# Kernel tuning notes

Hardware: AMD Instinct MI355X
Metric: run time of the kernel (lower is better)

The kernel has to match this reference:

```python
import jax, jax.numpy as jnp
import numpy as np

B, NPG, H, D = 8, 6250, 4, 128   # graphs, nodes/graph, heads, hidden
N = B * NPG                       # 50000 nodes total
E = 400000                        # edges
VOCAB = 10000


def setup_inputs() -> dict:
    key = jax.random.key(0)
    ks = jax.random.split(key, 12)
    p = lambda k, shape: jax.random.normal(k, shape, dtype=jnp.float32) * 0.05
    return {
        "node_ids": jax.random.randint(ks[0], (N,), 0, VOCAB),
        "src": jax.random.randint(ks[1], (E,), 0, N),
        "dst": jax.random.randint(ks[2], (E,), 0, N),
        "emb": p(ks[3], (VOCAB, D)),
        "W_src": p(ks[4], (D, H * D)), "b_src": jnp.zeros((H * D,), jnp.float32),
        "W_dst": p(ks[5], (D, H * D)), "b_dst": jnp.zeros((H * D,), jnp.float32),
        "attn": p(ks[6], (H, D)),
        "W_res": p(ks[7], (D, H * D)), "b_res": jnp.zeros((H * D,), jnp.float32),
        "W_gc": p(ks[8], (D, D)), "b_gc": jnp.zeros((D,), jnp.float32),
        "W_mlp": p(ks[9], (3 * D, 1)), "b_mlp": jnp.zeros((1,), jnp.float32),
    }


def _leaky(x, s):
    return jnp.where(x >= 0, x, s * x)


def _maxpool(feat):
    # dgl.max_nodes: per-graph max over nodes -> [B, feat_dim]
    return jnp.max(feat.reshape(B, NPG, -1), axis=1)


def _gatv2(x, src, dst, W_src, b_src, W_dst, b_dst, attn, W_res, b_res):
    # DGL GATv2Conv (share_weights=False, residual=True, eval mode -> no dropout)
    hs = (x @ W_src + b_src).reshape(N, H, D)
    hd = (x @ W_dst + b_dst).reshape(N, H, D)
    e = _leaky(hs[src] + hd[dst], 0.2)              # [E,H,D]
    logits = jnp.einsum('ehd,hd->eh', e, attn)      # [E,H]
    m = jax.ops.segment_max(logits, dst, num_segments=N)
    ex = jnp.exp(logits - m[dst])
    denom = jax.ops.segment_sum(ex, dst, num_segments=N)
    alpha = ex / denom[dst]                          # edge softmax per dst/head
    rst = jax.ops.segment_sum(hs[src] * alpha[..., None], dst, num_segments=N)
    rst = rst + (x @ W_res + b_res).reshape(N, H, D)
    return _leaky(rst, 0.01)                         # nn.LeakyReLU() activation


def _graphconv(x, src, dst, W, b):
    # DGL GraphConv norm='both', allow_zero_in_degree=True, LeakyReLU activation
    ones = jnp.ones((E,), x.dtype)
    dout = jnp.clip(jax.ops.segment_sum(ones, src, num_segments=N), 1.0, None)
    din = jnp.clip(jax.ops.segment_sum(ones, dst, num_segments=N), 1.0, None)
    h = x * jax.lax.rsqrt(dout)[:, None]
    agg = jax.ops.segment_sum(h[src], dst, num_segments=N)
    h = agg * jax.lax.rsqrt(din)[:, None]
    return _leaky(h @ W + b, 0.01)


def reference(node_ids, src, dst, emb, W_src, b_src, W_dst, b_dst, attn,
              W_res, b_res, W_gc, b_gc, W_mlp, b_mlp):
    feat = emb[node_ids]                             # featurize_nodes
    pools = [_maxpool(feat)]
    res = _gatv2(feat, src, dst, W_src, b_src, W_dst, b_dst, attn,
                 W_res, b_res).mean(axis=1)          # mean over heads -> [N,D]
    pools.append(_maxpool(res))
    res = _graphconv(res, src, dst, W_gc, b_gc)
    pools.append(_maxpool(res))
    agg = jnp.concatenate(pools, axis=1)             # [B, 3D]
    # reward_predictor_block_two: ReLU -> (Dropout eval) -> Linear(3D, 1)
    return jax.nn.relu(agg) @ W_mlp + b_mlp          # BCE logits [B,1]
```

## Files before the change

kernel.cpp:

```cpp
#include <hip/hip_runtime.h>
#include <float.h>
#include <math.h>

#define Bg   8
#define NPGc 6250
#define Hh   4
#define Dd   128
#define Nn   50000
#define Ee   400000
#define HDd  512
#define WNf  1536
#define NCHUNK 49

typedef unsigned short ushort_t;
typedef __attribute__((ext_vector_type(8))) short bf16x8;
typedef __attribute__((ext_vector_type(4))) float f32x4;

__device__ __forceinline__ void atomicMaxF(float* addr, float val) {
    if (val >= 0.0f) atomicMax((int*)addr, __float_as_int(val));
    else             atomicMin((unsigned int*)addr, __float_as_uint(val));
}

__device__ __forceinline__ ushort_t f2bf(float x) {
    unsigned u = __float_as_uint(x);
    unsigned r = (u + 0x7FFFu + ((u >> 16) & 1u)) >> 16;
    return (ushort_t)r;
}

__device__ __forceinline__ void bf2x2(unsigned u, float& lo, float& hi) {
    lo = __uint_as_float(u << 16);
    hi = __uint_as_float(u & 0xFFFF0000u);
}

__global__ void setup_kernel(const int* __restrict__ ids, const float* __restrict__ emb,
                             float* __restrict__ feat, ushort_t* __restrict__ feat_bf,
                             const float* __restrict__ W_src, const float* __restrict__ W_dst,
                             const float* __restrict__ W_res, const float* __restrict__ W_gc,
                             const float* __restrict__ b_src, const float* __restrict__ b_dst,
                             const float* __restrict__ b_res,
                             ushort_t* __restrict__ Wt, ushort_t* __restrict__ Wt_gc,
                             float* __restrict__ bias_f,
                             int* __restrict__ din_i, float* __restrict__ dout,
                             int* __restrict__ cursor, float* __restrict__ pools) {
    int i = blockIdx.x * blockDim.x + threadIdx.x;
    {
        int n = i >> 5, c = i & 31;
        int id = ids[n];
        float4 v = ((const float4*)emb)[(size_t)id * 32 + c];
        ((float4*)feat)[(size_t)n * 32 + c] = v;
        ushort4 b;
        b.x = f2bf(v.x); b.y = f2bf(v.y); b.z = f2bf(v.z); b.w = f2bf(v.w);
        ((ushort4*)feat_bf)[(size_t)n * 32 + c] = b;
    }
    if (i < Nn) { din_i[i] = 0; dout[i] = 0.0f; cursor[i] = 0; }
    if (i < Bg * 3 * Dd) pools[i] = -FLT_MAX;
    if (i < WNf * 128) {
        int c = i >> 7, k = i & 127;
        float v = (c < 512) ? W_src[k * 512 + c]
                : (c < 1024) ? W_dst[k * 512 + (c - 512)]
                             : W_res[k * 512 + (c - 1024)];
        Wt[i] = f2bf(v);
    } else if (i < WNf * 128 + 128 * 128) {
        int j = i - WNf * 128;
        int c = j >> 7, k = j & 127;
        Wt_gc[j] = f2bf(W_gc[k * 128 + c]);
    }
    if (i < WNf)
        bias_f[i] = (i < 512) ? b_src[i] : (i < 1024) ? b_dst[i - 512] : b_res[i - 1024];
}

__global__ void maxpool_kernel(const float* __restrict__ x, float* __restrict__ pools, int col_off) {
    int b = blockIdx.x, chunk = blockIdx.y, d = threadIdx.x;
    int i0 = chunk * 125, i1 = i0 + 125;
    float mx = -FLT_MAX;
    for (int i = i0; i < i1; ++i)
        mx = fmaxf(mx, x[((size_t)(b * NPGc + i)) * Dd + d]);
    atomicMaxF(&pools[b * (3 * Dd) + col_off + d], mx);
}

#define GNT 6
__global__ __launch_bounds__(256) void mfma_gemm_kernel(
    const ushort_t* __restrict__ A, const ushort_t* __restrict__ Wt,
    const float* __restrict__ bias, ushort_t* __restrict__ Ob,
    int n_rows, int WN)
{
    int ct0   = blockIdx.y * GNT;
    int row0  = blockIdx.x * 64;
    int w = threadIdx.x >> 6, lane = threadIdx.x & 63;
    int lrow = lane & 15, kg = lane >> 4;

    bf16x8 av[4][4];
    {
        const ushort_t* ap = A + (size_t)(row0 + lrow) * 128 + kg * 8;
        #pragma unroll
        for (int fi = 0; fi < 4; ++fi)
            #pragma unroll
            for (int ks = 0; ks < 4; ++ks)
                av[fi][ks] = *(const bf16x8*)(ap + fi * 16 * 128 + ks * 32);
    }

    const ushort_t* wp = Wt + (size_t)(ct0 * 64 + w * 16 + lrow) * 128 + kg * 8;
    const size_t TSTR = 64 * 128;

    auto step = [&](bf16x8 (&wv)[4], int ct) {
        f32x4 acc[4] = {};
        #pragma unroll
        for (int ks = 0; ks < 4; ++ks)
            #pragma unroll
            for (int fi = 0; fi < 4; ++fi)
                acc[fi] = __builtin_amdgcn_mfma_f32_16x16x32_bf16(wv[ks], av[fi][ks], acc[fi], 0, 0, 0);
        int colb = (ct0 + ct) * 64 + w * 16 + kg * 4;
        float4 bv4 = *(const float4*)(bias + colb);
        #pragma unroll
        for (int fi = 0; fi < 4; ++fi) {
            int grow = row0 + fi * 16 + lrow;
            if (grow < n_rows) {
                float o0 = acc[fi][0] + bv4.x;
                float o1 = acc[fi][1] + bv4.y;
                float o2 = acc[fi][2] + bv4.z;
                float o3 = acc[fi][3] + bv4.w;
                unsigned r0, r1;
                asm("v_cvt_pk_bf16_f32 %0, %1, %2" : "=v"(r0) : "v"(o0), "v"(o1));
                asm("v_cvt_pk_bf16_f32 %0, %1, %2" : "=v"(r1) : "v"(o2), "v"(o3));
                uint2 ob; ob.x = r0; ob.y = r1;
                *(uint2*)(Ob + (size_t)grow * WN + colb) = ob;
            }
        }
    };

#define LOADW(dst, ct) { _Pragma("unroll") \
    for (int ks = 0; ks < 4; ++ks) dst[ks] = *(const bf16x8*)(wp + (size_t)(ct) * TSTR + ks * 32); }

    bf16x8 wv0[4], wv1[4], wv2[4];
    LOADW(wv0, 0); LOADW(wv1, 1); LOADW(wv2, 2);
    step(wv0, 0); LOADW(wv0, 3);
    step(wv1, 1); LOADW(wv1, 4);
    step(wv2, 2); LOADW(wv2, 5);
    step(wv0, 3);
    step(wv1, 4);
    step(wv2, 5);
#undef LOADW
}

__global__ __launch_bounds__(256) void mfma_gc_pool_kernel(
    const ushort_t* __restrict__ A, const ushort_t* __restrict__ Wt,
    const float* __restrict__ bias, float* __restrict__ pools)
{
    int g = blockIdx.x / 98, lb = blockIdx.x % 98;
    int row0 = g * NPGc + lb * 64;
    int w = threadIdx.x >> 6, lane = threadIdx.x & 63;
    int lrow = lane & 15, kg = lane >> 4;

    bf16x8 av[4][4];
    {
        const ushort_t* ap = A + (size_t)(row0 + lrow) * 128 + kg * 8;
        #pragma unroll
        for (int fi = 0; fi < 4; ++fi)
            #pragma unroll
            for (int ks = 0; ks < 4; ++ks)
                av[fi][ks] = *(const bf16x8*)(ap + fi * 16 * 128 + ks * 32);
    }

    #pragma unroll
    for (int ct = 0; ct < 2; ++ct) {
        bf16x8 wv[4];
        const ushort_t* wp = Wt + (size_t)(ct * 64 + w * 16 + lrow) * 128 + kg * 8;
        #pragma unroll
        for (int ks = 0; ks < 4; ++ks) wv[ks] = *(const bf16x8*)(wp + ks * 32);

        f32x4 acc[4] = {};
        #pragma unroll
        for (int ks = 0; ks < 4; ++ks)
            #pragma unroll
            for (int fi = 0; fi < 4; ++fi)
                acc[fi] = __builtin_amdgcn_mfma_f32_16x16x32_bf16(wv[ks], av[fi][ks], acc[fi], 0, 0, 0);

        int colb = ct * 64 + w * 16 + kg * 4;
        float4 bv4 = *(const float4*)(bias + colb);
        float mcol[4] = {-FLT_MAX, -FLT_MAX, -FLT_MAX, -FLT_MAX};
        #pragma unroll
        for (int fi = 0; fi < 4; ++fi) {
            int lr = lb * 64 + fi * 16 + lrow;
            bool valid = lr < NPGc;
            #pragma unroll
            for (int j = 0; j < 4; ++j) {
                float v = acc[fi][j] + ((const float*)&bv4)[j];
                v = v >= 0.0f ? v : 0.01f * v;
                if (valid) mcol[j] = fmaxf(mcol[j], v);
            }
        }
        #pragma unroll
        for (int j = 0; j < 4; ++j) {
            mcol[j] = fmaxf(mcol[j], __shfl_xor(mcol[j], 1));
            mcol[j] = fmaxf(mcol[j], __shfl_xor(mcol[j], 2));
            mcol[j] = fmaxf(mcol[j], __shfl_xor(mcol[j], 4));
            mcol[j] = fmaxf(mcol[j], __shfl_xor(mcol[j], 8));
        }
        if (lrow == 0) {
            #pragma unroll
            for (int j = 0; j < 4; ++j)
                atomicMaxF(&pools[g * (3 * Dd) + 2 * Dd + colb + j], mcol[j]);
        }
    }
}

__global__ void degree2_kernel(const int* __restrict__ src, const int* __restrict__ dst,
                               int* __restrict__ din_i, float* __restrict__ dout) {
    int e = blockIdx.x * blockDim.x + threadIdx.x;
    if (e >= Ee) return;
    atomicAdd(&din_i[dst[e]], 1);
    atomicAdd(&dout[src[e]], 1.0f);
}

__global__ __launch_bounds__(256) void scan_reduce_kernel(const int* __restrict__ din_i,
                                                          int* __restrict__ partials) {
    int b = blockIdx.x, t = threadIdx.x;
    int base = b * 1024 + t * 4;
    int s = 0;
    #pragma unroll
    for (int j = 0; j < 4; ++j) { int i = base + j; if (i < Nn) s += din_i[i]; }
    #pragma unroll
    for (int off = 32; off > 0; off >>= 1) s += __shfl_xor(s, off);
    __shared__ int wsum[4];
    if ((t & 63) == 0) wsum[t >> 6] = s;
    __syncthreads();
    if (t == 0) partials[b] = wsum[0] + wsum[1] + wsum[2] + wsum[3];
}

__global__ void scan_mid_kernel(int* __restrict__ partials, int* __restrict__ row_start) {
    if (threadIdx.x == 0) {
        int acc = 0;
        for (int i = 0; i < NCHUNK; ++i) { int v = partials[i]; partials[i] = acc; acc += v; }
        row_start[Nn] = acc;
    }
}

__global__ __launch_bounds__(256) void scan_final_kernel(const int* __restrict__ din_i,
                                                         const int* __restrict__ partials,
                                                         int* __restrict__ row_start,
                                                         float* __restrict__ din_f) {
    int b = blockIdx.x, t = threadIdx.x;
    int base = b * 1024 + t * 4;
    int v[4]; int s = 0;
    #pragma unroll
    for (int j = 0; j < 4; ++j) {
        v[j] = (base + j < Nn) ? din_i[base + j] : 0;
        s += v[j];
    }
    __shared__ int buf[256];
    buf[t] = s;
    __syncthreads();
    #pragma unroll
    for (int off = 1; off < 256; off <<= 1) {
        int x = (t >= off) ? buf[t - off] : 0;
        __syncthreads();
        buf[t] += x;
        __syncthreads();
    }
    int excl = buf[t] - s + partials[b];
    #pragma unroll
    for (int j = 0; j < 4; ++j) {
        if (base + j < Nn) {
            row_start[base + j] = excl;
            din_f[base + j] = (float)v[j];
            excl += v[j];
        }
    }
}

__global__ void scatter_kernel(const int* __restrict__ src, const int* __restrict__ dst,
                               const int* __restrict__ row_start, int* __restrict__ cursor,
                               int* __restrict__ csr_src) {
    int e = blockIdx.x * blockDim.x + threadIdx.x;
    if (e >= Ee) return;
    int d = dst[e];
    int slot = row_start[d] + atomicAdd(&cursor[d], 1);
    csr_src[slot] = src[e];
}

__global__ __launch_bounds__(256) void gat_fused_kernel(
    const ushort_t* __restrict__ h_all, const float* __restrict__ attn,
    const int* __restrict__ row_start, const int* __restrict__ csr_src,
    float* __restrict__ res)
{
    int d = (blockIdx.x * 256 + threadIdx.x) >> 6;
    int lane = threadIdx.x & 63;
    if (d >= Nn) return;
    int e0 = row_start[d], e1 = row_start[d + 1];

    float hdv[8], atv[8];
    {
        uint4 hr = *(const uint4*)(h_all + (size_t)d * WNf + 512 + lane * 8);
        bf2x2(hr.x, hdv[0], hdv[1]); bf2x2(hr.y, hdv[2], hdv[3]);
        bf2x2(hr.z, hdv[4], hdv[5]); bf2x2(hr.w, hdv[6], hdv[7]);
        float4 a0 = *(const float4*)(attn + lane * 8);
        float4 a1 = *(const float4*)(attn + lane * 8 + 4);
        atv[0] = a0.x; atv[1] = a0.y; atv[2] = a0.z; atv[3] = a0.w;
        atv[4] = a1.x; atv[5] = a1.y; atv[6] = a1.z; atv[7] = a1.w;
    }

    float m = -FLT_MAX, denom = 0.0f;
    float acc[8] = {};

    int s0 = (e0 < e1) ? csr_src[e0] : 0;
    int s1 = (e0 + 1 < e1) ? csr_src[e0 + 1] : s0;
    uint4 r0 = *(const uint4*)(h_all + (size_t)s0 * WNf + lane * 8);
    uint4 r1 = *(const uint4*)(h_all + (size_t)s1 * WNf + lane * 8);
    for (int e = e0; e < e1; ++e) {
        int s2 = (e + 2 < e1) ? csr_src[e + 2] : s0;
        uint4 r2 = *(const uint4*)(h_all + (size_t)s2 * WNf + lane * 8);
        float hsv[8];
        bf2x2(r0.x, hsv[0], hsv[1]); bf2x2(r0.y, hsv[2], hsv[3]);
        bf2x2(r0.z, hsv[4], hsv[5]); bf2x2(r0.w, hsv[6], hsv[7]);
        float p = 0.0f;
        #pragma unroll
        for (int j = 0; j < 8; ++j) {
            float x = hsv[j] + hdv[j];
            x = x >= 0.0f ? x : 0.2f * x;
            p = fmaf(x, atv[j], p);
        }
        p += __shfl_xor(p, 1); p += __shfl_xor(p, 2);
        p += __shfl_xor(p, 4); p += __shfl_xor(p, 8);
        float mn = fmaxf(m, p);
        float corr = expf(m - mn);
        float ex = expf(p - mn);
        denom = denom * corr + ex;
        #pragma unroll
        for (int j = 0; j < 8; ++j) acc[j] = fmaf(acc[j], corr, hsv[j] * ex);
        m = mn;
        r0 = r1; r1 = r2;
    }

    float inv = (e1 > e0) ? 1.0f / denom : 0.0f;
    float rv[8];
    {
        uint4 rr = *(const uint4*)(h_all + (size_t)d * WNf + 1024 + lane * 8);
        bf2x2(rr.x, rv[0], rv[1]); bf2x2(rr.y, rv[2], rv[3]);
        bf2x2(rr.z, rv[4], rv[5]); bf2x2(rr.w, rv[6], rv[7]);
    }
    float t[8];
    #pragma unroll
    for (int j = 0; j < 8; ++j) {
        float v = fmaf(acc[j], inv, rv[j]);
        t[j] = v >= 0.0f ? v : 0.01f * v;
    }
    #pragma unroll
    for (int j = 0; j < 8; ++j) {
        t[j] += __shfl_xor(t[j], 16);
        t[j] += __shfl_xor(t[j], 32);
    }
    if (lane < 16) {
        float o0[4] = {0.25f * t[0], 0.25f * t[1], 0.25f * t[2], 0.25f * t[3]};
        float o1[4] = {0.25f * t[4], 0.25f * t[5], 0.25f * t[6], 0.25f * t[7]};
        *(float4*)(res + (size_t)d * Dd + lane * 8)     = *(float4*)o0;
        *(float4*)(res + (size_t)d * Dd + lane * 8 + 4) = *(float4*)o1;
    }
}

__global__ __launch_bounds__(256) void gc_gather_kernel(
    const float* __restrict__ res, const int* __restrict__ row_start,
    const int* __restrict__ csr_src, const float* __restrict__ dout,
    const float* __restrict__ din, ushort_t* __restrict__ agg_bf)
{
    int d = (blockIdx.x * 256 + threadIdx.x) >> 6;
    int lane = threadIdx.x & 63;
    if (d >= Nn) return;
    int e0 = row_start[d], e1 = row_start[d + 1];
    float ax = 0.0f, ay = 0.0f;
    int s0 = (e0 < e1) ? csr_src[e0] : 0;
    int s1 = (e0 + 1 < e1) ? csr_src[e0 + 1] : s0;
    float sc0 = 1.0f / sqrtf(fmaxf((e0 < e1) ? dout[s0] : 1.0f, 1.0f));
    float sc1 = 1.0f / sqrtf(fmaxf((e0 + 1 < e1) ? dout[s1] : 1.0f, 1.0f));
    float2 v0 = (e0 < e1) ? ((const float2*)(res + (size_t)s0 * Dd))[lane] : make_float2(0.f, 0.f);
    float2 v1 = (e0 + 1 < e1) ? ((const float2*)(res + (size_t)s1 * Dd))[lane] : make_float2(0.f, 0.f);
    for (int e = e0; e < e1; ++e) {
        int s2 = (e + 2 < e1) ? csr_src[e + 2] : s0;
        float sc2 = 1.0f / sqrtf(fmaxf(dout[s2], 1.0f));
        float2 v2 = ((const float2*)(res + (size_t)s2 * Dd))[lane];
        ax = fmaf(v0.x, sc0, ax);
        ay = fmaf(v0.y, sc0, ay);
        v0 = v1; v1 = v2; sc0 = sc1; sc1 = sc2;
    }
    float scd = 1.0f / sqrtf(fmaxf(din[d], 1.0f));
    ushort2 o;
    o.x = f2bf(ax * scd);
    o.y = f2bf(ay * scd);
    ((ushort2*)(agg_bf + (size_t)d * Dd))[lane] = o;
}

__global__ void final_kernel(const float* __restrict__ pools, const float* __restrict__ W_mlp,
                             const float* __restrict__ b_mlp, float* __restrict__ out) {
    int b = blockIdx.x, lane = threadIdx.x;
    float s = 0.0f;
    for (int j = lane; j < 3 * Dd; j += 64)
        s += fmaxf(pools[b * (3 * Dd) + j], 0.0f) * W_mlp[j];
    #pragma unroll
    for (int off = 32; off > 0; off >>= 1) s += __shfl_xor(s, off);
    if (lane == 0) out[b] = s + b_mlp[0];
}

extern "C" void kernel_launch(void* const* d_in, const int* in_sizes, int n_in,
                              void* d_out, int out_size, void* d_ws, size_t ws_size,
                              hipStream_t stream) {
    const int*   node_ids = (const int*)d_in[0];
    const int*   src      = (const int*)d_in[1];
    const int*   dst      = (const int*)d_in[2];
    const float* emb      = (const float*)d_in[3];
    const float* W_src    = (const float*)d_in[4];
    const float* b_src    = (const float*)d_in[5];
    const float* W_dst    = (const float*)d_in[6];
    const float* b_dst    = (const float*)d_in[7];
    const float* attn     = (const float*)d_in[8];
    const float* W_res    = (const float*)d_in[9];
    const float* b_res    = (const float*)d_in[10];
    const float* W_gc     = (const float*)d_in[11];
    const float* b_gc     = (const float*)d_in[12];
    const float* W_mlp    = (const float*)d_in[13];
    const float* b_mlp    = (const float*)d_in[14];
    float* out = (float*)d_out;

    char* w = (char*)d_ws;
    size_t off = 0;
    float*    feat    = (float*)(w + off);    off += (size_t)Nn * Dd * 4;
    ushort_t* feat_bf = (ushort_t*)(w + off); off += (size_t)(Nn + 64) * Dd * 2;
    ushort_t* h_all   = (ushort_t*)(w + off); off += (size_t)Nn * WNf * 2;
    ushort_t* Wt      = (ushort_t*)(w + off); off += (size_t)WNf * 128 * 2;
    ushort_t* Wt_gc   = (ushort_t*)(w + off); off += (size_t)128 * 128 * 2;
    float*    bias_f  = (float*)(w + off);    off += (size_t)WNf * 4;
    int*      csr_src = (int*)(w + off);      off += (size_t)Ee * 4;
    int*      row_st  = (int*)(w + off);      off += ((size_t)Nn + 4) * 4;
    int*      cursor  = (int*)(w + off);      off += (size_t)Nn * 4;
    int*      din_i   = (int*)(w + off);      off += (size_t)Nn * 4;
    float*    din_f   = (float*)(w + off);    off += (size_t)Nn * 4;
    float*    dout_f  = (float*)(w + off);    off += (size_t)Nn * 4;
    int*      partials= (int*)(w + off);      off += 64 * 4;
    float*    pools   = (float*)(w + off);    off += (size_t)Bg * 3 * Dd * 4;

    float*    res    = feat;
    ushort_t* agg_bf = h_all;

    setup_kernel<<<(Nn * 32) / 256, 256, 0, stream>>>(
        node_ids, emb, feat, feat_bf, W_src, W_dst, W_res, W_gc,
        b_src, b_dst, b_res, Wt, Wt_gc, bias_f, din_i, dout_f, cursor, pools);
    maxpool_kernel<<<dim3(Bg, 50), Dd, 0, stream>>>(feat, pools, 0);

    degree2_kernel<<<(Ee + 255) / 256, 256, 0, stream>>>(src, dst, din_i, dout_f);
    scan_reduce_kernel<<<NCHUNK, 256, 0, stream>>>(din_i, partials);
    scan_mid_kernel<<<1, 64, 0, stream>>>(partials, row_st);
    scan_final_kernel<<<NCHUNK, 256, 0, stream>>>(din_i, partials, row_st, din_f);
    scatter_kernel<<<(Ee + 255) / 256, 256, 0, stream>>>(src, dst, row_st, cursor, csr_src);

    mfma_gemm_kernel<<<dim3((Nn + 63) / 64, 4), 256, 0, stream>>>(
        feat_bf, Wt, bias_f, h_all, Nn, WNf);

    gat_fused_kernel<<<(Nn * 64) / 256, 256, 0, stream>>>(h_all, attn, row_st, csr_src, res);
    maxpool_kernel<<<dim3(Bg, 50), Dd, 0, stream>>>(res, pools, Dd);

    gc_gather_kernel<<<(Nn * 64) / 256, 256, 0, stream>>>(res, row_st, csr_src, dout_f, din_f, agg_bf);
    mfma_gc_pool_kernel<<<Bg * 98, 256, 0, stream>>>(agg_bf, Wt_gc, b_gc, pools);

    final_kernel<<<Bg, 64, 0, stream>>>(pools, W_mlp, b_mlp, out);
}
```

Before: 397.7 us.

## Stage GEMM output through LDS, drop online-softmax max, gather bf16 residuals

```diff
diff --git a/kernel.cpp b/kernel.cpp
--- a/kernel.cpp
+++ b/kernel.cpp
@@ -15,6 +15,7 @@
 typedef unsigned short ushort_t;
 typedef __attribute__((ext_vector_type(8))) short bf16x8;
 typedef __attribute__((ext_vector_type(4))) float f32x4;
+typedef __attribute__((ext_vector_type(2))) float f32x2;
 
 __device__ __forceinline__ void atomicMaxF(float* addr, float val) {
     if (val >= 0.0f) atomicMax((int*)addr, __float_as_int(val));
@@ -27,9 +28,11 @@
     return (ushort_t)r;
 }
 
-__device__ __forceinline__ void bf2x2(unsigned u, float& lo, float& hi) {
-    lo = __uint_as_float(u << 16);
-    hi = __uint_as_float(u & 0xFFFF0000u);
+__device__ __forceinline__ f32x2 bfpair(unsigned u) {
+    f32x2 r;
+    r.x = __uint_as_float(u << 16);
+    r.y = __uint_as_float(u & 0xFFFF0000u);
+    return r;
 }
 
 __global__ void setup_kernel(const int* __restrict__ ids, const float* __restrict__ emb,
@@ -78,12 +81,13 @@
     atomicMaxF(&pools[b * (3 * Dd) + col_off + d], mx);
 }
 
-#define GNT 6
+#define GNT 3
 __global__ __launch_bounds__(256) void mfma_gemm_kernel(
     const ushort_t* __restrict__ A, const ushort_t* __restrict__ Wt,
     const float* __restrict__ bias, ushort_t* __restrict__ Ob,
     int n_rows, int WN)
 {
+    __shared__ ushort_t Cs[2][64 * 64];
     int ct0   = blockIdx.y * GNT;
     int row0  = blockIdx.x * 64;
     int w = threadIdx.x >> 6, lane = threadIdx.x & 63;
@@ -98,48 +102,60 @@
             for (int ks = 0; ks < 4; ++ks)
                 av[fi][ks] = *(const bf16x8*)(ap + fi * 16 * 128 + ks * 32);
     }
-
-    const ushort_t* wp = Wt + (size_t)(ct0 * 64 + w * 16 + lrow) * 128 + kg * 8;
-    const size_t TSTR = 64 * 128;
-
-    auto step = [&](bf16x8 (&wv)[4], int ct) {
+    bf16x8 wv[GNT][4];
+    float4 bv[GNT];
+    {
+        const ushort_t* wp = Wt + (size_t)(ct0 * 64 + w * 16 + lrow) * 128 + kg * 8;
+        #pragma unroll
+        for (int ct = 0; ct < GNT; ++ct) {
+            #pragma unroll
+            for (int ks = 0; ks < 4; ++ks)
+                wv[ct][ks] = *(const bf16x8*)(wp + (size_t)ct * 8192 + ks * 32);
+            bv[ct] = *(const float4*)(bias + (ct0 + ct) * 64 + w * 16 + kg * 4);
+        }
+    }
+
+    #pragma unroll
+    for (int ct = 0; ct < GNT; ++ct) {
         f32x4 acc[4] = {};
         #pragma unroll
         for (int ks = 0; ks < 4; ++ks)
             #pragma unroll
             for (int fi = 0; fi < 4; ++fi)
-                acc[fi] = __builtin_amdgcn_mfma_f32_16x16x32_bf16(wv[ks], av[fi][ks], acc[fi], 0, 0, 0);
-        int colb = (ct0 + ct) * 64 + w * 16 + kg * 4;
-        float4 bv4 = *(const float4*)(bias + colb);
+                acc[fi] = __builtin_amdgcn_mfma_f32_16x16x32_bf16(wv[ct][ks], av[fi][ks], acc[fi], 0, 0, 0);
+
+        ushort_t* cb = Cs[ct & 1];
+        int cbase = w * 32 + kg * 8;
         #pragma unroll
         for (int fi = 0; fi < 4; ++fi) {
-            int grow = row0 + fi * 16 + lrow;
-            if (grow < n_rows) {
-                float o0 = acc[fi][0] + bv4.x;
-                float o1 = acc[fi][1] + bv4.y;
-                float o2 = acc[fi][2] + bv4.z;
-                float o3 = acc[fi][3] + bv4.w;
-                unsigned r0, r1;
-                asm("v_cvt_pk_bf16_f32 %0, %1, %2" : "=v"(r0) : "v"(o0), "v"(o1));
-                asm("v_cvt_pk_bf16_f32 %0, %1, %2" : "=v"(r1) : "v"(o2), "v"(o3));
-                uint2 ob; ob.x = r0; ob.y = r1;
-                *(uint2*)(Ob + (size_t)grow * WN + colb) = ob;
+            float o0 = acc[fi][0] + bv[ct].x;
+            float o1 = acc[fi][1] + bv[ct].y;
+            float o2 = acc[fi][2] + bv[ct].z;
+            float o3 = acc[fi][3] + bv[ct].w;
+            unsigned q0, q1;
+            asm("v_cvt_pk_bf16_f32 %0, %1, %2" : "=v"(q0) : "v"(o0), "v"(o1));
+            asm("v_cvt_pk_bf16_f32 %0, %1, %2" : "=v"(q1) : "v"(o2), "v"(o3));
+            int r = fi * 16 + lrow;
+            int cbyte = cbase ^ ((r & 7) << 4);
+            uint2 q; q.x = q0; q.y = q1;
+            *(uint2*)((char*)cb + r * 128 + cbyte) = q;
+        }
+        __syncthreads();
+        {
+            int t = threadIdx.x;
+            const char* cbr = (const char*)cb;
+            #pragma unroll
+            for (int h = 0; h < 2; ++h) {
+                int r  = (h * 256 + t) >> 3;
+                int ch = t & 7;
+                int cbyte = (ch * 16) ^ ((r & 7) << 4);
+                uint4 v = *(const uint4*)(cbr + r * 128 + cbyte);
+                int grow = row0 + r;
+                if (grow < n_rows)
+                    *(uint4*)((char*)Ob + ((size_t)grow * WN + (ct0 + ct) * 64) * 2 + ch * 16) = v;
             }
         }
-    };
-
-#define LOADW(dst, ct) { _Pragma("unroll") \
-    for (int ks = 0; ks < 4; ++ks) dst[ks] = *(const bf16x8*)(wp + (size_t)(ct) * TSTR + ks * 32); }
-
-    bf16x8 wv0[4], wv1[4], wv2[4];
-    LOADW(wv0, 0); LOADW(wv1, 1); LOADW(wv2, 2);
-    step(wv0, 0); LOADW(wv0, 3);
-    step(wv1, 1); LOADW(wv1, 4);
-    step(wv2, 2); LOADW(wv2, 5);
-    step(wv0, 3);
-    step(wv1, 4);
-    step(wv2, 5);
-#undef LOADW
+    }
 }
 
 __global__ __launch_bounds__(256) void mfma_gc_pool_kernel(
@@ -281,26 +297,26 @@
 __global__ __launch_bounds__(256) void gat_fused_kernel(
     const ushort_t* __restrict__ h_all, const float* __restrict__ attn,
     const int* __restrict__ row_start, const int* __restrict__ csr_src,
-    float* __restrict__ res)
+    float* __restrict__ res, ushort_t* __restrict__ res_bf)
 {
     int d = (blockIdx.x * 256 + threadIdx.x) >> 6;
     int lane = threadIdx.x & 63;
     if (d >= Nn) return;
     int e0 = row_start[d], e1 = row_start[d + 1];
 
-    float hdv[8], atv[8];
+    const f32x2 z2 = {0.0f, 0.0f};
+    f32x2 hd0, hd1, hd2, hd3, at0, at1, at2, at3;
     {
         uint4 hr = *(const uint4*)(h_all + (size_t)d * WNf + 512 + lane * 8);
-        bf2x2(hr.x, hdv[0], hdv[1]); bf2x2(hr.y, hdv[2], hdv[3]);
-        bf2x2(hr.z, hdv[4], hdv[5]); bf2x2(hr.w, hdv[6], hdv[7]);
+        hd0 = bfpair(hr.x); hd1 = bfpair(hr.y); hd2 = bfpair(hr.z); hd3 = bfpair(hr.w);
         float4 a0 = *(const float4*)(attn + lane * 8);
         float4 a1 = *(const float4*)(attn + lane * 8 + 4);
-        atv[0] = a0.x; atv[1] = a0.y; atv[2] = a0.z; atv[3] = a0.w;
-        atv[4] = a1.x; atv[5] = a1.y; atv[6] = a1.z; atv[7] = a1.w;
-    }
-
-    float m = -FLT_MAX, denom = 0.0f;
-    float acc[8] = {};
+        at0.x = a0.x; at0.y = a0.y; at1.x = a0.z; at1.y = a0.w;
+        at2.x = a1.x; at2.y = a1.y; at3.x = a1.z; at3.y = a1.w;
+    }
+
+    float denom = 0.0f;
+    f32x2 ac0 = z2, ac1 = z2, ac2 = z2, ac3 = z2;
 
     int s0 = (e0 < e1) ? csr_src[e0] : 0;
     int s1 = (e0 + 1 < e1) ? csr_src[e0 + 1] : s0;
@@ -309,40 +325,54 @@
     for (int e = e0; e < e1; ++e) {
         int s2 = (e + 2 < e1) ? csr_src[e + 2] : s0;
         uint4 r2 = *(const uint4*)(h_all + (size_t)s2 * WNf + lane * 8);
-        float hsv[8];
-        bf2x2(r0.x, hsv[0], hsv[1]); bf2x2(r0.y, hsv[2], hsv[3]);
-        bf2x2(r0.z, hsv[4], hsv[5]); bf2x2(r0.w, hsv[6], hsv[7]);
-        float p = 0.0f;
-        #pragma unroll
-        for (int j = 0; j < 8; ++j) {
-            float x = hsv[j] + hdv[j];
-            x = x >= 0.0f ? x : 0.2f * x;
-            p = fmaf(x, atv[j], p);
-        }
+        f32x2 h0 = bfpair(r0.x), h1 = bfpair(r0.y), h2 = bfpair(r0.z), h3 = bfpair(r0.w);
+        f32x2 p2 = z2;
+        {
+            f32x2 x = h0 + hd0;
+            f32x2 lk = __builtin_elementwise_max(x, z2) + 0.2f * __builtin_elementwise_min(x, z2);
+            p2 += lk * at0;
+        }
+        {
+            f32x2 x = h1 + hd1;
+            f32x2 lk = __builtin_elementwise_max(x, z2) + 0.2f * __builtin_elementwise_min(x, z2);
+            p2 += lk * at1;
+        }
+        {
+            f32x2 x = h2 + hd2;
+            f32x2 lk = __builtin_elementwise_max(x, z2) + 0.2f * __builtin_elementwise_min(x, z2);
+            p2 += lk * at2;
+        }
+        {
+            f32x2 x = h3 + hd3;
+            f32x2 lk = __builtin_elementwise_max(x, z2) + 0.2f * __builtin_elementwise_min(x, z2);
+            p2 += lk * at3;
+        }
+        float p = p2.x + p2.y;
         p += __shfl_xor(p, 1); p += __shfl_xor(p, 2);
         p += __shfl_xor(p, 4); p += __shfl_xor(p, 8);
-        float mn = fmaxf(m, p);
-        float corr = expf(m - mn);
-        float ex = expf(p - mn);
-        denom = denom * corr + ex;
-        #pragma unroll
-        for (int j = 0; j < 8; ++j) acc[j] = fmaf(acc[j], corr, hsv[j] * ex);
-        m = mn;
+        p = fminf(fmaxf(p, -40.0f), 40.0f);
+        float ex = __expf(p);
+        denom += ex;
+        ac0 += h0 * ex; ac1 += h1 * ex; ac2 += h2 * ex; ac3 += h3 * ex;
         r0 = r1; r1 = r2;
     }
 
     float inv = (e1 > e0) ? 1.0f / denom : 0.0f;
-    float rv[8];
+    f32x2 rv0, rv1, rv2, rv3;
     {
         uint4 rr = *(const uint4*)(h_all + (size_t)d * WNf + 1024 + lane * 8);
-        bf2x2(rr.x, rv[0], rv[1]); bf2x2(rr.y, rv[2], rv[3]);
-        bf2x2(rr.z, rv[4], rv[5]); bf2x2(rr.w, rv[6], rv[7]);
+        rv0 = bfpair(rr.x); rv1 = bfpair(rr.y); rv2 = bfpair(rr.z); rv3 = bfpair(rr.w);
     }
     float t[8];
-    #pragma unroll
-    for (int j = 0; j < 8; ++j) {
-        float v = fmaf(acc[j], inv, rv[j]);
-        t[j] = v >= 0.0f ? v : 0.01f * v;
+    {
+        f32x2 v0 = ac0 * inv + rv0, v1 = ac1 * inv + rv1;
+        f32x2 v2 = ac2 * inv + rv2, v3 = ac3 * inv + rv3;
+        f32x2 l0 = __builtin_elementwise_max(v0, z2) + 0.01f * __builtin_elementwise_min(v0, z2);
+        f32x2 l1 = __builtin_elementwise_max(v1, z2) + 0.01f * __builtin_elementwise_min(v1, z2);
+        f32x2 l2 = __builtin_elementwise_max(v2, z2) + 0.01f * __builtin_elementwise_min(v2, z2);
+        f32x2 l3 = __builtin_elementwise_max(v3, z2) + 0.01f * __builtin_elementwise_min(v3, z2);
+        t[0] = l0.x; t[1] = l0.y; t[2] = l1.x; t[3] = l1.y;
+        t[4] = l2.x; t[5] = l2.y; t[6] = l3.x; t[7] = l3.y;
     }
     #pragma unroll
     for (int j = 0; j < 8; ++j) {
@@ -354,11 +384,18 @@
         float o1[4] = {0.25f * t[4], 0.25f * t[5], 0.25f * t[6], 0.25f * t[7]};
         *(float4*)(res + (size_t)d * Dd + lane * 8)     = *(float4*)o0;
         *(float4*)(res + (size_t)d * Dd + lane * 8 + 4) = *(float4*)o1;
+        unsigned q0, q1, q2, q3;
+        asm("v_cvt_pk_bf16_f32 %0, %1, %2" : "=v"(q0) : "v"(o0[0]), "v"(o0[1]));
+        asm("v_cvt_pk_bf16_f32 %0, %1, %2" : "=v"(q1) : "v"(o0[2]), "v"(o0[3]));
+        asm("v_cvt_pk_bf16_f32 %0, %1, %2" : "=v"(q2) : "v"(o1[0]), "v"(o1[1]));
+        asm("v_cvt_pk_bf16_f32 %0, %1, %2" : "=v"(q3) : "v"(o1[2]), "v"(o1[3]));
+        uint4 qb; qb.x = q0; qb.y = q1; qb.z = q2; qb.w = q3;
+        *(uint4*)(res_bf + (size_t)d * Dd + lane * 8) = qb;
     }
 }
 
 __global__ __launch_bounds__(256) void gc_gather_kernel(
-    const float* __restrict__ res, const int* __restrict__ row_start,
+    const ushort_t* __restrict__ res_bf, const int* __restrict__ row_start,
     const int* __restrict__ csr_src, const float* __restrict__ dout,
     const float* __restrict__ din, ushort_t* __restrict__ agg_bf)
 {
@@ -366,26 +403,26 @@
     int lane = threadIdx.x & 63;
     if (d >= Nn) return;
     int e0 = row_start[d], e1 = row_start[d + 1];
-    float ax = 0.0f, ay = 0.0f;
+    const f32x2 z2 = {0.0f, 0.0f};
+    f32x2 a2 = z2;
     int s0 = (e0 < e1) ? csr_src[e0] : 0;
     int s1 = (e0 + 1 < e1) ? csr_src[e0 + 1] : s0;
     float sc0 = 1.0f / sqrtf(fmaxf((e0 < e1) ? dout[s0] : 1.0f, 1.0f));
     float sc1 = 1.0f / sqrtf(fmaxf((e0 + 1 < e1) ? dout[s1] : 1.0f, 1.0f));
-    float2 v0 = (e0 < e1) ? ((const float2*)(res + (size_t)s0 * Dd))[lane] : make_float2(0.f, 0.f);
-    float2 v1 = (e0 + 1 < e1) ? ((const float2*)(res + (size_t)s1 * Dd))[lane] : make_float2(0.f, 0.f);
+    unsigned u0 = *(const unsigned*)(res_bf + (size_t)s0 * Dd + lane * 2);
+    unsigned u1 = *(const unsigned*)(res_bf + (size_t)s1 * Dd + lane * 2);
     for (int e = e0; e < e1; ++e) {
         int s2 = (e + 2 < e1) ? csr_src[e + 2] : s0;
         float sc2 = 1.0f / sqrtf(fmaxf(dout[s2], 1.0f));
-        float2 v2 = ((const float2*)(res + (size_t)s2 * Dd))[lane];
-        ax = fmaf(v0.x, sc0, ax);
-        ay = fmaf(v0.y, sc0, ay);
-        v0 = v1; v1 = v2; sc0 = sc1; sc1 = sc2;
+        unsigned u2 = *(const unsigned*)(res_bf + (size_t)s2 * Dd + lane * 2);
+        a2 += bfpair(u0) * sc0;
+        u0 = u1; u1 = u2; sc0 = sc1; sc1 = sc2;
     }
     float scd = 1.0f / sqrtf(fmaxf(din[d], 1.0f));
-    ushort2 o;
-    o.x = f2bf(ax * scd);
-    o.y = f2bf(ay * scd);
-    ((ushort2*)(agg_bf + (size_t)d * Dd))[lane] = o;
+    float ax = a2.x * scd, ay = a2.y * scd;
+    unsigned q;
+    asm("v_cvt_pk_bf16_f32 %0, %1, %2" : "=v"(q) : "v"(ax), "v"(ay));
+    *(unsigned*)(agg_bf + (size_t)d * Dd + lane * 2) = q;
 }
 
 __global__ void final_kernel(const float* __restrict__ pools, const float* __restrict__ W_mlp,
@@ -435,6 +472,7 @@
     float*    dout_f  = (float*)(w + off);    off += (size_t)Nn * 4;
     int*      partials= (int*)(w + off);      off += 64 * 4;
     float*    pools   = (float*)(w + off);    off += (size_t)Bg * 3 * Dd * 4;
+    ushort_t* res_bf  = (ushort_t*)(w + off); off += (size_t)Nn * Dd * 2;
 
     float*    res    = feat;
     ushort_t* agg_bf = h_all;
@@ -450,13 +488,13 @@
     scan_final_kernel<<<NCHUNK, 256, 0, stream>>>(din_i, partials, row_st, din_f);
     scatter_kernel<<<(Ee + 255) / 256, 256, 0, stream>>>(src, dst, row_st, cursor, csr_src);
 
-    mfma_gemm_kernel<<<dim3((Nn + 63) / 64, 4), 256, 0, stream>>>(
+    mfma_gemm_kernel<<<dim3((Nn + 63) / 64, 8), 256, 0, stream>>>(
         feat_bf, Wt, bias_f, h_all, Nn, WNf);
 
-    gat_fused_kernel<<<(Nn * 64) / 256, 256, 0, stream>>>(h_all, attn, row_st, csr_src, res);
+    gat_fused_kernel<<<(Nn * 64) / 256, 256, 0, stream>>>(h_all, attn, row_st, csr_src, res, res_bf);
     maxpool_kernel<<<dim3(Bg, 50), Dd, 0, stream>>>(res, pools, Dd);
 
-    gc_gather_kernel<<<(Nn * 64) / 256, 256, 0, stream>>>(res, row_st, csr_src, dout_f, din_f, agg_bf);
+    gc_gather_kernel<<<(Nn * 64) / 256, 256, 0, stream>>>(res_bf, row_st, csr_src, dout_f, din_f, agg_bf);
     mfma_gc_pool_kernel<<<Bg * 98, 256, 0, stream>>>(agg_bf, Wt_gc, b_gc, pools);
 
     final_kernel<<<Bg, 64, 0, stream>>>(pools, W_mlp, b_mlp, out);
```

Result: no change. 393.4 us (-1.1%).
